# Kernel optimization log

Measured on AMD Instinct MI355X. Metric: run time of the kernel, lower is better.

## Reference

```python
import jax, jax.numpy as jnp
import numpy as np

B, C, T, H, W = 4, 256, 16, 16, 16
C2 = C // 2  # 128


def setup_inputs() -> dict:
    key = jax.random.key(0)
    ks = jax.random.split(key, 12)
    s = 1.0 / np.sqrt(C)
    return {
        "X": jax.random.normal(ks[0], (B, C, T, H, W), dtype=jnp.float32),
        "pe": jax.random.uniform(ks[1], (C, T, H, W), dtype=jnp.float32),
        "task_q": jax.random.uniform(ks[2], (C2, T, H, W), dtype=jnp.float32),
        "task_k": jax.random.uniform(ks[3], (C2, T, H, W), dtype=jnp.float32),
        "task_v": jax.random.uniform(ks[4], (C2, T, H, W), dtype=jnp.float32),
        "Wq": jax.random.normal(ks[5], (C2, C), dtype=jnp.float32) * s,
        "bq": jnp.zeros((C2,), dtype=jnp.float32),
        "Wk": jax.random.normal(ks[6], (C2, C), dtype=jnp.float32) * s,
        "bk": jnp.zeros((C2,), dtype=jnp.float32),
        "Wv": jax.random.normal(ks[7], (C2, C), dtype=jnp.float32) * s,
        "bv": jnp.zeros((C2,), dtype=jnp.float32),
        "Wo": jax.random.normal(ks[8], (C, C2), dtype=jnp.float32) * s,
    }


def reference(X, pe, task_q, task_k, task_v, Wq, bq, Wk, bk, Wv, bv, Wo):
    b, c, t, h, w = X.shape
    c2 = Wq.shape[0]
    n = t * h * w
    Xp = X + pe  # broadcast [C,T,H,W] over batch

    def proj(Wm, bm, task):
        # 1x1x1 Conv3d == channel contraction; add bias and per-task offset
        y = jnp.einsum('bcthw,oc->bothw', Xp, Wm)
        return y + bm[:, None, None, None] + task  # [B,C2,T,H,W]

    q = proj(Wq, bq, task_q).reshape(b, c2, n).transpose(0, 2, 1)  # [B,N,C2]
    k = proj(Wk, bk, task_k).reshape(b, c2, n)                     # [B,C2,N]
    sim = jnp.matmul(q, k)                                         # [B,N,N]
    v = proj(Wv, bv, task_v).reshape(b, c2, n).transpose(0, 2, 1)  # [B,N,C2]
    # NOTE: original torch code computes softmax(sim) but then multiplies by
    # the RAW similarity matrix (softmax output is dead code). Faithful math:
    out = jnp.matmul(sim, v)                                       # [B,N,C2]
    # torch .reshape of contiguous [B,N,C2] -> [B,C2,T,H,W] (layout reinterpret)
    out = out.reshape(b, c2, t, h, w)
    out = jnp.einsum('bcthw,oc->bothw', out, Wo)  # out_conv, no bias
    return out + X
```

## Files before the change

kernel.cpp:

```cpp
#include <hip/hip_runtime.h>
#include <cstddef>

#define BB 4
#define CCH 256
#define C2 128
#define NN 4096
#define PM 384
#define KVS 32

typedef __attribute__((ext_vector_type(8))) short short8v;
typedef __attribute__((ext_vector_type(4))) short short4v;
typedef __attribute__((ext_vector_type(4))) float f32x4;

static __device__ __forceinline__ short f2bf(float f) {
    union { float f; unsigned u; } c; c.f = f;
    unsigned r = (c.u + 0x7FFFu + ((c.u >> 16) & 1u)) >> 16;
    return (short)r;
}

__global__ __launch_bounds__(256) void k_pack(
    const float* __restrict__ Wq, const float* __restrict__ bq,
    const float* __restrict__ Wk, const float* __restrict__ bk,
    const float* __restrict__ Wv, const float* __restrict__ bv,
    short* __restrict__ wpackh, float* __restrict__ bpack)
{
    const int m = blockIdx.x;
    const int c = threadIdx.x;
    const float* w; const float* bs; int mm;
    if (m < C2)        { w = Wq; bs = bq; mm = m; }
    else if (m < 2*C2) { w = Wk; bs = bk; mm = m - C2; }
    else               { w = Wv; bs = bv; mm = m - 2*C2; }
    wpackh[m * CCH + c] = f2bf(w[mm * CCH + c]);
    if (c == 0) bpack[m] = bs[mm];
}

#define LROW 40
__global__ __launch_bounds__(256) void k_projm(
    const float* __restrict__ X, const float* __restrict__ pe,
    const float* __restrict__ tq, const float* __restrict__ tk,
    const float* __restrict__ tv,
    const short* __restrict__ wpackh, const float* __restrict__ bpack,
    float* __restrict__ qkv)
{
    __shared__ short As[128 * LROW];
    __shared__ short Bs[128 * LROW];
    const int b  = blockIdx.z;
    const int m0 = blockIdx.y * 128;
    const int n0 = blockIdx.x * 128;
    const int tid  = threadIdx.x;
    const int wave = tid >> 6;
    const int lane = tid & 63;
    const int lr = lane & 15, lg = lane >> 4;
    const int wm = wave >> 1, wn = wave & 1;
    const float* __restrict__ Xb = X + (size_t)b * CCH * NN;

    const int am  = tid >> 1;
    const int akb = tid & 1;
    const int cq = tid >> 5;
    const int nq = tid & 31;

    f32x4 acc[4][4];
#pragma unroll
    for (int i = 0; i < 4; ++i)
#pragma unroll
        for (int j = 0; j < 4; ++j) acc[i][j] = (f32x4){0.f, 0.f, 0.f, 0.f};

    for (int k0 = 0; k0 < CCH; k0 += 32) {
        {
            const size_t gsrc = (size_t)(m0 + am) * CCH + k0 + akb * 16;
            *(short8v*)&As[am * LROW + akb * 16] =
                *(const short8v*)&wpackh[gsrc];
            *(short8v*)&As[am * LROW + akb * 16 + 8] =
                *(const short8v*)&wpackh[gsrc + 8];
        }
        short sreg[4][4];
#pragma unroll
        for (int j = 0; j < 4; ++j) {
            const int c = k0 + cq * 4 + j;
            const size_t g = (size_t)c * NN + n0 + nq * 4;
            float4 x4 = *(const float4*)&Xb[g];
            float4 p4 = *(const float4*)&pe[g];
            sreg[j][0] = f2bf(x4.x + p4.x);
            sreg[j][1] = f2bf(x4.y + p4.y);
            sreg[j][2] = f2bf(x4.z + p4.z);
            sreg[j][3] = f2bf(x4.w + p4.w);
        }
#pragma unroll
        for (int i = 0; i < 4; ++i) {
            short4v v; v.x = sreg[0][i]; v.y = sreg[1][i]; v.z = sreg[2][i]; v.w = sreg[3][i];
            *(short4v*)&Bs[(nq * 4 + i) * LROW + cq * 4] = v;
        }
        __syncthreads();
        short8v a[4], bfr[4];
#pragma unroll
        for (int fm = 0; fm < 4; ++fm)
            a[fm] = *(const short8v*)&As[(wm * 64 + fm * 16 + lr) * LROW + lg * 8];
#pragma unroll
        for (int fn = 0; fn < 4; ++fn)
            bfr[fn] = *(const short8v*)&Bs[(wn * 64 + fn * 16 + lr) * LROW + lg * 8];
#pragma unroll
        for (int fm = 0; fm < 4; ++fm)
#pragma unroll
            for (int fn = 0; fn < 4; ++fn)
                acc[fm][fn] = __builtin_amdgcn_mfma_f32_16x16x32_bf16(
                    a[fm], bfr[fn], acc[fm][fn], 0, 0, 0);
        __syncthreads();
    }

    const int sel = m0 >> 7;
    const float* __restrict__ task = (sel == 0) ? tq : ((sel == 1) ? tk : tv);
#pragma unroll
    for (int fm = 0; fm < 4; ++fm) {
#pragma unroll
        for (int r = 0; r < 4; ++r) {
            const int m = m0 + wm * 64 + fm * 16 + lg * 4 + r;
            const float bia = bpack[m];
            const int mr = m & (C2 - 1);
#pragma unroll
            for (int fn = 0; fn < 4; ++fn) {
                const int n = n0 + wn * 64 + fn * 16 + lr;
                const float t = task[(size_t)mr * NN + n];
                qkv[((size_t)b * PM + m) * NN + n] = acc[fm][fn][r] + bia + t;
            }
        }
    }
}

__global__ __launch_bounds__(256) void k_kv(
    const float* __restrict__ qkv, float* __restrict__ Mpart)
{
    __shared__ float Ks[64][128];
    __shared__ float Vs[64][128];
    const int b = blockIdx.y;
    const int s = blockIdx.x;
    const int tid = threadIdx.x;
    const int r = tid >> 1;
    const int nb = (tid & 1) * 32;
    const int ti = tid >> 4, tj = tid & 15;
    const float* __restrict__ Kg = qkv + ((size_t)b * PM + C2) * NN;
    const float* __restrict__ Vg = qkv + ((size_t)b * PM + 2 * C2) * NN;
    float acc[8][8];
#pragma unroll
    for (int i = 0; i < 8; ++i)
#pragma unroll
        for (int j = 0; j < 8; ++j) acc[i][j] = 0.f;

    for (int half = 0; half < 2; ++half) {
        const int n0 = s * 128 + half * 64;
#pragma unroll
        for (int q = 0; q < 8; ++q) {
            const int nn = nb + q * 4;
            float4 kv = *(const float4*)&Kg[(size_t)r * NN + n0 + nn];
            Ks[nn+0][r] = kv.x; Ks[nn+1][r] = kv.y; Ks[nn+2][r] = kv.z; Ks[nn+3][r] = kv.w;
            float4 vv = *(const float4*)&Vg[(size_t)r * NN + n0 + nn];
            Vs[nn+0][r] = vv.x; Vs[nn+1][r] = vv.y; Vs[nn+2][r] = vv.z; Vs[nn+3][r] = vv.w;
        }
        __syncthreads();
        for (int nn = 0; nn < 64; ++nn) {
            float4 a0 = *(const float4*)&Ks[nn][ti * 8];
            float4 a1 = *(const float4*)&Ks[nn][ti * 8 + 4];
            float4 b0 = *(const float4*)&Vs[nn][tj * 8];
            float4 b1 = *(const float4*)&Vs[nn][tj * 8 + 4];
            float a[8] = {a0.x, a0.y, a0.z, a0.w, a1.x, a1.y, a1.z, a1.w};
            float v[8] = {b0.x, b0.y, b0.z, b0.w, b1.x, b1.y, b1.z, b1.w};
#pragma unroll
            for (int ii = 0; ii < 8; ++ii)
#pragma unroll
                for (int jj = 0; jj < 8; ++jj)
                    acc[ii][jj] += a[ii] * v[jj];
        }
        __syncthreads();
    }
    float* __restrict__ Mp = Mpart + ((size_t)b * KVS + s) * C2 * C2;
#pragma unroll
    for (int ii = 0; ii < 8; ++ii) {
        const int row = ti * 8 + ii;
        float4 o0, o1;
        o0.x = acc[ii][0]; o0.y = acc[ii][1]; o0.z = acc[ii][2]; o0.w = acc[ii][3];
        o1.x = acc[ii][4]; o1.y = acc[ii][5]; o1.z = acc[ii][6]; o1.w = acc[ii][7];
        *(float4*)&Mp[row * C2 + tj * 8]     = o0;
        *(float4*)&Mp[row * C2 + tj * 8 + 4] = o1;
    }
}

__global__ __launch_bounds__(256) void k_kvred(
    const float* __restrict__ Mpart, float* __restrict__ Mb)
{
    const int b = blockIdx.y;
    const int o = (blockIdx.x * 256 + threadIdx.x) * 4;
    const float* __restrict__ p = Mpart + (size_t)b * KVS * C2 * C2 + o;
    float4 acc;
    acc.x = 0.f; acc.y = 0.f; acc.z = 0.f; acc.w = 0.f;
#pragma unroll 4
    for (int s = 0; s < KVS; ++s) {
        float4 v = *(const float4*)&p[(size_t)s * C2 * C2];
        acc.x += v.x; acc.y += v.y; acc.z += v.z; acc.w += v.w;
    }
    *(float4*)&Mb[(size_t)b * C2 * C2 + o] = acc;
}

__global__ __launch_bounds__(256) void k_qm(
    const float* __restrict__ qkv, const float* __restrict__ Mb,
    float* __restrict__ out3)
{
    __shared__ float Qs[128][64];
    __shared__ float Ms[128][64];
    const int b = blockIdx.z;
    const int nbase = blockIdx.x * 64;
    const int jbase = blockIdx.y * 64;
    const int tid = threadIdx.x;
    const int r = tid >> 1;
    const int cb = (tid & 1) * 32;
    const float* __restrict__ Qg = qkv + (size_t)b * PM * NN;
    const float* __restrict__ Mg = Mb + (size_t)b * C2 * C2;
#pragma unroll
    for (int q = 0; q < 8; ++q) {
        const int cc = cb + q * 4;
        *(float4*)&Qs[r][cc] = *(const float4*)&Qg[(size_t)r * NN + nbase + cc];
        *(float4*)&Ms[r][cc] = *(const float4*)&Mg[r * C2 + jbase + cc];
    }
    __syncthreads();
    const int tn = tid >> 4, tj = tid & 15;
    float acc[4][4];
#pragma unroll
    for (int i = 0; i < 4; ++i)
#pragma unroll
        for (int j = 0; j < 4; ++j) acc[i][j] = 0.f;
    for (int i = 0; i < 128; ++i) {
        float4 a  = *(const float4*)&Qs[i][tn * 4];
        float4 m4 = *(const float4*)&Ms[i][tj * 4];
        float av[4] = {a.x, a.y, a.z, a.w};
        float mv[4] = {m4.x, m4.y, m4.z, m4.w};
#pragma unroll
        for (int ii = 0; ii < 4; ++ii)
#pragma unroll
            for (int jj = 0; jj < 4; ++jj)
                acc[ii][jj] += av[ii] * mv[jj];
    }
#pragma unroll
    for (int ii = 0; ii < 4; ++ii) {
        float4 o;
        o.x = acc[ii][0]; o.y = acc[ii][1]; o.z = acc[ii][2]; o.w = acc[ii][3];
        *(float4*)&out3[((size_t)b * NN + nbase + tn * 4 + ii) * C2 + jbase + tj * 4] = o;
    }
}

__global__ __launch_bounds__(256) void k_final(
    const float* __restrict__ out3, const float* __restrict__ Wo,
    const float* __restrict__ X, float* __restrict__ out)
{
    __shared__ float Ds[64][128];
    __shared__ float Wos[64][128];
    const int g  = blockIdx.x;
    const int o0 = blockIdx.y * 128;
    const int b  = blockIdx.z;
    const int tid = threadIdx.x;
    const int to = tid >> 4, tj = tid & 15;
    float acc[8][8];
#pragma unroll
    for (int i = 0; i < 8; ++i)
#pragma unroll
        for (int j = 0; j < 8; ++j) acc[i][j] = 0.f;

    const float* __restrict__ O3 = out3 + (size_t)b * NN * C2;

    for (int ch = 0; ch < 2; ++ch) {
        const int c0 = ch * 64;
        {
            const int r  = tid >> 2;
            const int jb2 = (tid & 3) * 32;
#pragma unroll
            for (int q = 0; q < 8; ++q) {
                const int j = jb2 + q * 4;
                *(float4*)&Ds[r][j] =
                    *(const float4*)&O3[(size_t)((c0 + r) * 32 + g) * C2 + j];
            }
        }
        {
            const int o  = tid >> 1;
            const int cb2 = (tid & 1) * 32;
#pragma unroll
            for (int q = 0; q < 8; ++q) {
                const int cc = cb2 + q * 4;
                float4 w = *(const float4*)&Wo[(size_t)(o0 + o) * C2 + c0 + cc];
                Wos[cc+0][o] = w.x; Wos[cc+1][o] = w.y;
                Wos[cc+2][o] = w.z; Wos[cc+3][o] = w.w;
            }
        }
        __syncthreads();
#pragma unroll
        for (int cc = 0; cc < 64; ++cc) {
            float4 w0 = *(const float4*)&Wos[cc][to * 8];
            float4 w1 = *(const float4*)&Wos[cc][to * 8 + 4];
            float4 d0 = *(const float4*)&Ds[cc][tj * 8];
            float4 d1 = *(const float4*)&Ds[cc][tj * 8 + 4];
            float w[8] = {w0.x, w0.y, w0.z, w0.w, w1.x, w1.y, w1.z, w1.w};
            float d[8] = {d0.x, d0.y, d0.z, d0.w, d1.x, d1.y, d1.z, d1.w};
#pragma unroll
            for (int ii = 0; ii < 8; ++ii)
#pragma unroll
                for (int jj = 0; jj < 8; ++jj)
                    acc[ii][jj] += w[ii] * d[jj];
        }
        __syncthreads();
    }

    const float* __restrict__ Xb = X + (size_t)b * CCH * NN;
    float* __restrict__ Ob = out + (size_t)b * CCH * NN;
#pragma unroll
    for (int oo = 0; oo < 8; ++oo) {
        const int o = o0 + to * 8 + oo;
        const size_t base = (size_t)o * NN + g * 128 + tj * 8;
        float4 x0 = *(const float4*)&Xb[base];
        float4 x1 = *(const float4*)&Xb[base + 4];
        float4 r0, r1;
        r0.x = acc[oo][0] + x0.x; r0.y = acc[oo][1] + x0.y;
        r0.z = acc[oo][2] + x0.z; r0.w = acc[oo][3] + x0.w;
        r1.x = acc[oo][4] + x1.x; r1.y = acc[oo][5] + x1.y;
        r1.z = acc[oo][6] + x1.z; r1.w = acc[oo][7] + x1.w;
        *(float4*)&Ob[base]     = r0;
        *(float4*)&Ob[base + 4] = r1;
    }
}

extern "C" void kernel_launch(void* const* d_in, const int* in_sizes, int n_in,
                              void* d_out, int out_size, void* d_ws, size_t ws_size,
                              hipStream_t stream) {
    const float* X  = (const float*)d_in[0];
    const float* pe = (const float*)d_in[1];
    const float* tq = (const float*)d_in[2];
    const float* tk = (const float*)d_in[3];
    const float* tv = (const float*)d_in[4];
    const float* Wq = (const float*)d_in[5];
    const float* bq = (const float*)d_in[6];
    const float* Wk = (const float*)d_in[7];
    const float* bk = (const float*)d_in[8];
    const float* Wv = (const float*)d_in[9];
    const float* bv = (const float*)d_in[10];
    const float* Wo = (const float*)d_in[11];
    float* out = (float*)d_out;

    float* ws     = (float*)d_ws;
    float* bpack  = ws;
    short* wpackh = (short*)(ws + 512);
    float* qkv    = ws + 512 + 49152;
    float* Mbuf   = qkv + (size_t)BB * PM * NN;
    float* Mpart  = Mbuf + (size_t)BB * C2 * C2;
    float* out3   = Mpart;

    k_pack<<<dim3(PM), dim3(256), 0, stream>>>(Wq, bq, Wk, bk, Wv, bv, wpackh, bpack);
    k_projm<<<dim3(NN / 128, PM / 128, BB), dim3(256), 0, stream>>>(
        X, pe, tq, tk, tv, wpackh, bpack, qkv);
    k_kv<<<dim3(KVS, BB), dim3(256), 0, stream>>>(qkv, Mpart);
    k_kvred<<<dim3(16, BB), dim3(256), 0, stream>>>(Mpart, Mbuf);
    k_qm<<<dim3(NN / 64, 2, BB), dim3(256), 0, stream>>>(qkv, Mbuf, out3);
    k_final<<<dim3(32, 2, BB), dim3(256), 0, stream>>>(out3, Wo, X, out);
}
```

Measured before the change: 169.7 us.

## Store Q/K/V and intermediates in bf16 and use MFMA for K^T V, QM and output projection

The projection epilogue now writes bf16 Q (transposed to [N,C2]), K and V through a shared-memory staging tile instead of fp32 qkv. The K^T V, Q·M and Wo-projection kernels switch from fp32 FMA loops to bf16 MFMA instructions that read operands directly from global memory, and Wo is packed to bf16 in the pack kernel. The kv split count is halved, and the reduction writes a transposed bf16 M. This cuts memory traffic and moves the matmuls onto matrix cores, but adds bf16 rounding to intermediates and uses uncoalesced scalar gathers in k_final.

```diff
diff --git a/kernel.cpp b/kernel.cpp
--- a/kernel.cpp
+++ b/kernel.cpp
@@ -6,7 +6,7 @@
 #define C2 128
 #define NN 4096
 #define PM 384
-#define KVS 32
+#define KVS 16
 
 typedef __attribute__((ext_vector_type(8))) short short8v;
 typedef __attribute__((ext_vector_type(4))) short short4v;
@@ -22,28 +22,37 @@
     const float* __restrict__ Wq, const float* __restrict__ bq,
     const float* __restrict__ Wk, const float* __restrict__ bk,
     const float* __restrict__ Wv, const float* __restrict__ bv,
-    short* __restrict__ wpackh, float* __restrict__ bpack)
+    const float* __restrict__ Wo,
+    short* __restrict__ wpackh, float* __restrict__ bpack,
+    short* __restrict__ Woh)
 {
     const int m = blockIdx.x;
     const int c = threadIdx.x;
-    const float* w; const float* bs; int mm;
-    if (m < C2)        { w = Wq; bs = bq; mm = m; }
-    else if (m < 2*C2) { w = Wk; bs = bk; mm = m - C2; }
-    else               { w = Wv; bs = bv; mm = m - 2*C2; }
-    wpackh[m * CCH + c] = f2bf(w[mm * CCH + c]);
-    if (c == 0) bpack[m] = bs[mm];
+    if (m < PM) {
+        const float* w; const float* bs; int mm;
+        if (m < C2)        { w = Wq; bs = bq; mm = m; }
+        else if (m < 2*C2) { w = Wk; bs = bk; mm = m - C2; }
+        else               { w = Wv; bs = bv; mm = m - 2*C2; }
+        wpackh[m * CCH + c] = f2bf(w[mm * CCH + c]);
+        if (c == 0) bpack[m] = bs[mm];
+    } else {
+        const int o = m - PM;
+        if (c < C2) Woh[o * C2 + c] = f2bf(Wo[o * C2 + c]);
+    }
 }
 
 #define LROW 40
+#define TSP  136
 __global__ __launch_bounds__(256) void k_projm(
     const float* __restrict__ X, const float* __restrict__ pe,
     const float* __restrict__ tq, const float* __restrict__ tk,
     const float* __restrict__ tv,
     const short* __restrict__ wpackh, const float* __restrict__ bpack,
-    float* __restrict__ qkv)
-{
-    __shared__ short As[128 * LROW];
-    __shared__ short Bs[128 * LROW];
+    short* __restrict__ qt, short* __restrict__ kk, short* __restrict__ vv)
+{
+    __shared__ short smem[17408];
+    short* As = smem;
+    short* Bs = smem + 5120;
     const int b  = blockIdx.z;
     const int m0 = blockIdx.y * 128;
     const int n0 = blockIdx.x * 128;
@@ -56,8 +65,8 @@
 
     const int am  = tid >> 1;
     const int akb = tid & 1;
-    const int cq = tid >> 5;
-    const int nq = tid & 31;
+    const int cq  = tid >> 5;
+    const int nq  = tid & 31;
 
     f32x4 acc[4][4];
 #pragma unroll
@@ -68,10 +77,8 @@
     for (int k0 = 0; k0 < CCH; k0 += 32) {
         {
             const size_t gsrc = (size_t)(m0 + am) * CCH + k0 + akb * 16;
-            *(short8v*)&As[am * LROW + akb * 16] =
-                *(const short8v*)&wpackh[gsrc];
-            *(short8v*)&As[am * LROW + akb * 16 + 8] =
-                *(const short8v*)&wpackh[gsrc + 8];
+            *(short8v*)&As[am * LROW + akb * 16]     = *(const short8v*)&wpackh[gsrc];
+            *(short8v*)&As[am * LROW + akb * 16 + 8] = *(const short8v*)&wpackh[gsrc + 8];
         }
         short sreg[4][4];
 #pragma unroll
@@ -107,220 +114,230 @@
         __syncthreads();
     }
 
+    short* Ts = smem;
     const int sel = m0 >> 7;
-    const float* __restrict__ task = (sel == 0) ? tq : ((sel == 1) ? tk : tv);
-#pragma unroll
-    for (int fm = 0; fm < 4; ++fm) {
-#pragma unroll
-        for (int r = 0; r < 4; ++r) {
-            const int m = m0 + wm * 64 + fm * 16 + lg * 4 + r;
-            const float bia = bpack[m];
-            const int mr = m & (C2 - 1);
+    if (sel == 0) {
+#pragma unroll
+        for (int fm = 0; fm < 4; ++fm)
 #pragma unroll
             for (int fn = 0; fn < 4; ++fn) {
-                const int n = n0 + wn * 64 + fn * 16 + lr;
-                const float t = task[(size_t)mr * NN + n];
-                qkv[((size_t)b * PM + m) * NN + n] = acc[fm][fn][r] + bia + t;
+                const int n_l  = wn * 64 + fn * 16 + lr;
+                const int m_lb = wm * 64 + fm * 16 + lg * 4;
+                short4v v;
+#pragma unroll
+                for (int r = 0; r < 4; ++r) {
+                    const int m_l = m_lb + r;
+                    v[r] = f2bf(acc[fm][fn][r] + bpack[m_l]
+                                + tq[(size_t)m_l * NN + n0 + n_l]);
+                }
+                *(short4v*)&Ts[n_l * TSP + m_lb] = v;
             }
-        }
+        __syncthreads();
+        const int n_l = tid >> 1, half = tid & 1;
+        short* dst = qt + (size_t)b * NN * C2 + (size_t)(n0 + n_l) * C2 + half * 64;
+        const short* src = &Ts[n_l * TSP + half * 64];
+#pragma unroll
+        for (int q2 = 0; q2 < 8; ++q2)
+            *(short8v*)&dst[q2 * 8] = *(const short8v*)&src[q2 * 8];
+    } else {
+        const float* __restrict__ task = (sel == 1) ? tk : tv;
+        short* kv = (sel == 1) ? kk : vv;
+#pragma unroll
+        for (int fm = 0; fm < 4; ++fm)
+#pragma unroll
+            for (int fn = 0; fn < 4; ++fn) {
+                const int n_l = wn * 64 + fn * 16 + lr;
+#pragma unroll
+                for (int r = 0; r < 4; ++r) {
+                    const int m_l = wm * 64 + fm * 16 + lg * 4 + r;
+                    Ts[m_l * TSP + n_l] =
+                        f2bf(acc[fm][fn][r] + bpack[m0 + m_l]
+                             + task[(size_t)m_l * NN + n0 + n_l]);
+                }
+            }
+        __syncthreads();
+        const int m_l = tid >> 1, half = tid & 1;
+        short* dst = kv + (size_t)b * C2 * NN + (size_t)m_l * NN + n0 + half * 64;
+        const short* src = &Ts[m_l * TSP + half * 64];
+#pragma unroll
+        for (int q2 = 0; q2 < 8; ++q2)
+            *(short8v*)&dst[q2 * 8] = *(const short8v*)&src[q2 * 8];
     }
 }
 
 __global__ __launch_bounds__(256) void k_kv(
-    const float* __restrict__ qkv, float* __restrict__ Mpart)
-{
-    __shared__ float Ks[64][128];
-    __shared__ float Vs[64][128];
+    const short* __restrict__ kk, const short* __restrict__ vv,
+    float* __restrict__ Mpart)
+{
+    const int b = blockIdx.y, s = blockIdx.x;
+    const int tid = threadIdx.x;
+    const int wave = tid >> 6, lane = tid & 63;
+    const int lr = lane & 15, lg = lane >> 4;
+    const int wi = wave >> 1, wj = wave & 1;
+    const short* Kb = kk + (size_t)b * C2 * NN;
+    const short* Vb = vv + (size_t)b * C2 * NN;
+    const int nbase = s * 256;
+    f32x4 acc[4][4];
+#pragma unroll
+    for (int i = 0; i < 4; ++i)
+#pragma unroll
+        for (int j = 0; j < 4; ++j) acc[i][j] = (f32x4){0.f, 0.f, 0.f, 0.f};
+
+    for (int ks = 0; ks < 8; ++ks) {
+        const int nn = nbase + ks * 32 + lg * 8;
+        short8v a[4], bv8[4];
+#pragma unroll
+        for (int fi = 0; fi < 4; ++fi)
+            a[fi] = *(const short8v*)&Kb[(size_t)(wi * 64 + fi * 16 + lr) * NN + nn];
+#pragma unroll
+        for (int fj = 0; fj < 4; ++fj)
+            bv8[fj] = *(const short8v*)&Vb[(size_t)(wj * 64 + fj * 16 + lr) * NN + nn];
+#pragma unroll
+        for (int fi = 0; fi < 4; ++fi)
+#pragma unroll
+            for (int fj = 0; fj < 4; ++fj)
+                acc[fi][fj] = __builtin_amdgcn_mfma_f32_16x16x32_bf16(
+                    a[fi], bv8[fj], acc[fi][fj], 0, 0, 0);
+    }
+    float* Mp = Mpart + ((size_t)b * KVS + s) * C2 * C2;
+#pragma unroll
+    for (int fi = 0; fi < 4; ++fi)
+#pragma unroll
+        for (int fj = 0; fj < 4; ++fj) {
+            const int j = wj * 64 + fj * 16 + lr;
+#pragma unroll
+            for (int r = 0; r < 4; ++r) {
+                const int i = wi * 64 + fi * 16 + lg * 4 + r;
+                Mp[(size_t)i * C2 + j] = acc[fi][fj][r];
+            }
+        }
+}
+
+__global__ __launch_bounds__(256) void k_kvred(
+    const float* __restrict__ Mpart, short* __restrict__ Mt)
+{
     const int b = blockIdx.y;
-    const int s = blockIdx.x;
+    const int i = blockIdx.x * 16 + (threadIdx.x >> 4);
+    const int j0 = (threadIdx.x & 15) * 8;
+    const float* p = Mpart + (size_t)b * KVS * C2 * C2 + (size_t)i * C2 + j0;
+    float a8[8];
+#pragma unroll
+    for (int e = 0; e < 8; ++e) a8[e] = 0.f;
+    for (int s = 0; s < KVS; ++s) {
+        float4 v0 = *(const float4*)&p[(size_t)s * C2 * C2];
+        float4 v1 = *(const float4*)&p[(size_t)s * C2 * C2 + 4];
+        a8[0] += v0.x; a8[1] += v0.y; a8[2] += v0.z; a8[3] += v0.w;
+        a8[4] += v1.x; a8[5] += v1.y; a8[6] += v1.z; a8[7] += v1.w;
+    }
+    short* mt = Mt + (size_t)b * C2 * C2;
+#pragma unroll
+    for (int e = 0; e < 8; ++e)
+        mt[(size_t)(j0 + e) * C2 + i] = f2bf(a8[e]);
+}
+
+__global__ __launch_bounds__(256) void k_qm(
+    const short* __restrict__ qt, const short* __restrict__ Mt,
+    short* __restrict__ out3)
+{
+    const int b = blockIdx.y;
+    const int n0 = blockIdx.x * 128;
     const int tid = threadIdx.x;
-    const int r = tid >> 1;
-    const int nb = (tid & 1) * 32;
-    const int ti = tid >> 4, tj = tid & 15;
-    const float* __restrict__ Kg = qkv + ((size_t)b * PM + C2) * NN;
-    const float* __restrict__ Vg = qkv + ((size_t)b * PM + 2 * C2) * NN;
-    float acc[8][8];
-#pragma unroll
-    for (int i = 0; i < 8; ++i)
-#pragma unroll
-        for (int j = 0; j < 8; ++j) acc[i][j] = 0.f;
-
-    for (int half = 0; half < 2; ++half) {
-        const int n0 = s * 128 + half * 64;
-#pragma unroll
-        for (int q = 0; q < 8; ++q) {
-            const int nn = nb + q * 4;
-            float4 kv = *(const float4*)&Kg[(size_t)r * NN + n0 + nn];
-            Ks[nn+0][r] = kv.x; Ks[nn+1][r] = kv.y; Ks[nn+2][r] = kv.z; Ks[nn+3][r] = kv.w;
-            float4 vv = *(const float4*)&Vg[(size_t)r * NN + n0 + nn];
-            Vs[nn+0][r] = vv.x; Vs[nn+1][r] = vv.y; Vs[nn+2][r] = vv.z; Vs[nn+3][r] = vv.w;
-        }
-        __syncthreads();
-        for (int nn = 0; nn < 64; ++nn) {
-            float4 a0 = *(const float4*)&Ks[nn][ti * 8];
-            float4 a1 = *(const float4*)&Ks[nn][ti * 8 + 4];
-            float4 b0 = *(const float4*)&Vs[nn][tj * 8];
-            float4 b1 = *(const float4*)&Vs[nn][tj * 8 + 4];
-            float a[8] = {a0.x, a0.y, a0.z, a0.w, a1.x, a1.y, a1.z, a1.w};
-            float v[8] = {b0.x, b0.y, b0.z, b0.w, b1.x, b1.y, b1.z, b1.w};
-#pragma unroll
-            for (int ii = 0; ii < 8; ++ii)
-#pragma unroll
-                for (int jj = 0; jj < 8; ++jj)
-                    acc[ii][jj] += a[ii] * v[jj];
-        }
-        __syncthreads();
-    }
-    float* __restrict__ Mp = Mpart + ((size_t)b * KVS + s) * C2 * C2;
-#pragma unroll
-    for (int ii = 0; ii < 8; ++ii) {
-        const int row = ti * 8 + ii;
-        float4 o0, o1;
-        o0.x = acc[ii][0]; o0.y = acc[ii][1]; o0.z = acc[ii][2]; o0.w = acc[ii][3];
-        o1.x = acc[ii][4]; o1.y = acc[ii][5]; o1.z = acc[ii][6]; o1.w = acc[ii][7];
-        *(float4*)&Mp[row * C2 + tj * 8]     = o0;
-        *(float4*)&Mp[row * C2 + tj * 8 + 4] = o1;
-    }
-}
-
-__global__ __launch_bounds__(256) void k_kvred(
-    const float* __restrict__ Mpart, float* __restrict__ Mb)
-{
-    const int b = blockIdx.y;
-    const int o = (blockIdx.x * 256 + threadIdx.x) * 4;
-    const float* __restrict__ p = Mpart + (size_t)b * KVS * C2 * C2 + o;
-    float4 acc;
-    acc.x = 0.f; acc.y = 0.f; acc.z = 0.f; acc.w = 0.f;
-#pragma unroll 4
-    for (int s = 0; s < KVS; ++s) {
-        float4 v = *(const float4*)&p[(size_t)s * C2 * C2];
-        acc.x += v.x; acc.y += v.y; acc.z += v.z; acc.w += v.w;
-    }
-    *(float4*)&Mb[(size_t)b * C2 * C2 + o] = acc;
-}
-
-__global__ __launch_bounds__(256) void k_qm(
-    const float* __restrict__ qkv, const float* __restrict__ Mb,
-    float* __restrict__ out3)
-{
-    __shared__ float Qs[128][64];
-    __shared__ float Ms[128][64];
-    const int b = blockIdx.z;
-    const int nbase = blockIdx.x * 64;
-    const int jbase = blockIdx.y * 64;
-    const int tid = threadIdx.x;
-    const int r = tid >> 1;
-    const int cb = (tid & 1) * 32;
-    const float* __restrict__ Qg = qkv + (size_t)b * PM * NN;
-    const float* __restrict__ Mg = Mb + (size_t)b * C2 * C2;
-#pragma unroll
-    for (int q = 0; q < 8; ++q) {
-        const int cc = cb + q * 4;
-        *(float4*)&Qs[r][cc] = *(const float4*)&Qg[(size_t)r * NN + nbase + cc];
-        *(float4*)&Ms[r][cc] = *(const float4*)&Mg[r * C2 + jbase + cc];
-    }
-    __syncthreads();
-    const int tn = tid >> 4, tj = tid & 15;
-    float acc[4][4];
+    const int wave = tid >> 6, lane = tid & 63;
+    const int lr = lane & 15, lg = lane >> 4;
+    const int wj = wave >> 1, wn = wave & 1;
+    const short* Mb = Mt + (size_t)b * C2 * C2;
+    const short* Qb = qt + (size_t)b * NN * C2;
+    f32x4 acc[4][4];
 #pragma unroll
     for (int i = 0; i < 4; ++i)
 #pragma unroll
-        for (int j = 0; j < 4; ++j) acc[i][j] = 0.f;
-    for (int i = 0; i < 128; ++i) {
-        float4 a  = *(const float4*)&Qs[i][tn * 4];
-        float4 m4 = *(const float4*)&Ms[i][tj * 4];
-        float av[4] = {a.x, a.y, a.z, a.w};
-        float mv[4] = {m4.x, m4.y, m4.z, m4.w};
-#pragma unroll
-        for (int ii = 0; ii < 4; ++ii)
-#pragma unroll
-            for (int jj = 0; jj < 4; ++jj)
-                acc[ii][jj] += av[ii] * mv[jj];
-    }
-#pragma unroll
-    for (int ii = 0; ii < 4; ++ii) {
-        float4 o;
-        o.x = acc[ii][0]; o.y = acc[ii][1]; o.z = acc[ii][2]; o.w = acc[ii][3];
-        *(float4*)&out3[((size_t)b * NN + nbase + tn * 4 + ii) * C2 + jbase + tj * 4] = o;
-    }
+        for (int j = 0; j < 4; ++j) acc[i][j] = (f32x4){0.f, 0.f, 0.f, 0.f};
+
+    for (int ks = 0; ks < 4; ++ks) {
+        const int kb = ks * 32 + lg * 8;
+        short8v a[4], bq8[4];
+#pragma unroll
+        for (int fj = 0; fj < 4; ++fj)
+            a[fj] = *(const short8v*)&Mb[(size_t)(wj * 64 + fj * 16 + lr) * C2 + kb];
+#pragma unroll
+        for (int fn = 0; fn < 4; ++fn)
+            bq8[fn] = *(const short8v*)&Qb[(size_t)(n0 + wn * 64 + fn * 16 + lr) * C2 + kb];
+#pragma unroll
+        for (int fj = 0; fj < 4; ++fj)
+#pragma unroll
+            for (int fn = 0; fn < 4; ++fn)
+                acc[fj][fn] = __builtin_amdgcn_mfma_f32_16x16x32_bf16(
+                    a[fj], bq8[fn], acc[fj][fn], 0, 0, 0);
+    }
+    short* O3 = out3 + (size_t)b * NN * C2;
+#pragma unroll
+    for (int fj = 0; fj < 4; ++fj)
+#pragma unroll
+        for (int fn = 0; fn < 4; ++fn) {
+            const int n  = n0 + wn * 64 + fn * 16 + lr;
+            const int jb = wj * 64 + fj * 16 + lg * 4;
+            short4v v;
+#pragma unroll
+            for (int r = 0; r < 4; ++r) v[r] = f2bf(acc[fj][fn][r]);
+            *(short4v*)&O3[(size_t)n * C2 + jb] = v;
+        }
 }
 
 __global__ __launch_bounds__(256) void k_final(
-    const float* __restrict__ out3, const float* __restrict__ Wo,
+    const short* __restrict__ out3, const short* __restrict__ Woh,
     const float* __restrict__ X, float* __restrict__ out)
 {
-    __shared__ float Ds[64][128];
-    __shared__ float Wos[64][128];
     const int g  = blockIdx.x;
     const int o0 = blockIdx.y * 128;
     const int b  = blockIdx.z;
     const int tid = threadIdx.x;
-    const int to = tid >> 4, tj = tid & 15;
-    float acc[8][8];
-#pragma unroll
-    for (int i = 0; i < 8; ++i)
-#pragma unroll
-        for (int j = 0; j < 8; ++j) acc[i][j] = 0.f;
-
-    const float* __restrict__ O3 = out3 + (size_t)b * NN * C2;
-
-    for (int ch = 0; ch < 2; ++ch) {
-        const int c0 = ch * 64;
-        {
-            const int r  = tid >> 2;
-            const int jb2 = (tid & 3) * 32;
-#pragma unroll
-            for (int q = 0; q < 8; ++q) {
-                const int j = jb2 + q * 4;
-                *(float4*)&Ds[r][j] =
-                    *(const float4*)&O3[(size_t)((c0 + r) * 32 + g) * C2 + j];
+    const int wave = tid >> 6, lane = tid & 63;
+    const int lr = lane & 15, lg = lane >> 4;
+    const int wm = wave >> 1, wn = wave & 1;
+    const short* O3 = out3 + (size_t)b * NN * C2;
+    f32x4 acc[4][4];
+#pragma unroll
+    for (int i = 0; i < 4; ++i)
+#pragma unroll
+        for (int j = 0; j < 4; ++j) acc[i][j] = (f32x4){0.f, 0.f, 0.f, 0.f};
+
+    for (int ks = 0; ks < 4; ++ks) {
+        const int c0 = ks * 32;
+        short8v a[4], bb[4];
+#pragma unroll
+        for (int fm = 0; fm < 4; ++fm)
+            a[fm] = *(const short8v*)&Woh[(size_t)(o0 + wm * 64 + fm * 16 + lr) * C2
+                                          + c0 + lg * 8];
+#pragma unroll
+        for (int fn = 0; fn < 4; ++fn) {
+            const int pj = wn * 64 + fn * 16 + lr;
+            short8v t;
+#pragma unroll
+            for (int e = 0; e < 8; ++e)
+                t[e] = O3[(size_t)((c0 + lg * 8 + e) * 32 + g) * C2 + pj];
+            bb[fn] = t;
+        }
+#pragma unroll
+        for (int fm = 0; fm < 4; ++fm)
+#pragma unroll
+            for (int fn = 0; fn < 4; ++fn)
+                acc[fm][fn] = __builtin_amdgcn_mfma_f32_16x16x32_bf16(
+                    a[fm], bb[fn], acc[fm][fn], 0, 0, 0);
+    }
+    const float* Xb = X + (size_t)b * CCH * NN;
+    float* Ob = out + (size_t)b * CCH * NN;
+#pragma unroll
+    for (int fm = 0; fm < 4; ++fm)
+#pragma unroll
+        for (int fn = 0; fn < 4; ++fn) {
+            const int p  = g * 128 + wn * 64 + fn * 16 + lr;
+            const int ob = o0 + wm * 64 + fm * 16 + lg * 4;
+#pragma unroll
+            for (int r = 0; r < 4; ++r) {
+                const size_t ad = (size_t)(ob + r) * NN + p;
+                Ob[ad] = acc[fm][fn][r] + Xb[ad];
             }
         }
-        {
-            const int o  = tid >> 1;
-            const int cb2 = (tid & 1) * 32;
-#pragma unroll
-            for (int q = 0; q < 8; ++q) {
-                const int cc = cb2 + q * 4;
-                float4 w = *(const float4*)&Wo[(size_t)(o0 + o) * C2 + c0 + cc];
-                Wos[cc+0][o] = w.x; Wos[cc+1][o] = w.y;
-                Wos[cc+2][o] = w.z; Wos[cc+3][o] = w.w;
-            }
-        }
-        __syncthreads();
-#pragma unroll
-        for (int cc = 0; cc < 64; ++cc) {
-            float4 w0 = *(const float4*)&Wos[cc][to * 8];
-            float4 w1 = *(const float4*)&Wos[cc][to * 8 + 4];
-            float4 d0 = *(const float4*)&Ds[cc][tj * 8];
-            float4 d1 = *(const float4*)&Ds[cc][tj * 8 + 4];
-            float w[8] = {w0.x, w0.y, w0.z, w0.w, w1.x, w1.y, w1.z, w1.w};
-            float d[8] = {d0.x, d0.y, d0.z, d0.w, d1.x, d1.y, d1.z, d1.w};
-#pragma unroll
-            for (int ii = 0; ii < 8; ++ii)
-#pragma unroll
-                for (int jj = 0; jj < 8; ++jj)
-                    acc[ii][jj] += w[ii] * d[jj];
-        }
-        __syncthreads();
-    }
-
-    const float* __restrict__ Xb = X + (size_t)b * CCH * NN;
-    float* __restrict__ Ob = out + (size_t)b * CCH * NN;
-#pragma unroll
-    for (int oo = 0; oo < 8; ++oo) {
-        const int o = o0 + to * 8 + oo;
-        const size_t base = (size_t)o * NN + g * 128 + tj * 8;
-        float4 x0 = *(const float4*)&Xb[base];
-        float4 x1 = *(const float4*)&Xb[base + 4];
-        float4 r0, r1;
-        r0.x = acc[oo][0] + x0.x; r0.y = acc[oo][1] + x0.y;
-        r0.z = acc[oo][2] + x0.z; r0.w = acc[oo][3] + x0.w;
-        r1.x = acc[oo][4] + x1.x; r1.y = acc[oo][5] + x1.y;
-        r1.z = acc[oo][6] + x1.z; r1.w = acc[oo][7] + x1.w;
-        *(float4*)&Ob[base]     = r0;
-        *(float4*)&Ob[base + 4] = r1;
-    }
 }
 
 extern "C" void kernel_launch(void* const* d_in, const int* in_sizes, int n_in,
@@ -343,16 +360,20 @@
     float* ws     = (float*)d_ws;
     float* bpack  = ws;
     short* wpackh = (short*)(ws + 512);
-    float* qkv    = ws + 512 + 49152;
-    float* Mbuf   = qkv + (size_t)BB * PM * NN;
-    float* Mpart  = Mbuf + (size_t)BB * C2 * C2;
-    float* out3   = Mpart;
-
-    k_pack<<<dim3(PM), dim3(256), 0, stream>>>(Wq, bq, Wk, bk, Wv, bv, wpackh, bpack);
-    k_projm<<<dim3(NN / 128, PM / 128, BB), dim3(256), 0, stream>>>(
-        X, pe, tq, tk, tv, wpackh, bpack, qkv);
-    k_kv<<<dim3(KVS, BB), dim3(256), 0, stream>>>(qkv, Mpart);
-    k_kvred<<<dim3(16, BB), dim3(256), 0, stream>>>(Mpart, Mbuf);
-    k_qm<<<dim3(NN / 64, 2, BB), dim3(256), 0, stream>>>(qkv, Mbuf, out3);
-    k_final<<<dim3(32, 2, BB), dim3(256), 0, stream>>>(out3, Wo, X, out);
-}
+    short* Woh    = (short*)(ws + 512 + 49152);
+    short* qt     = (short*)(ws + 512 + 49152 + 16384);
+    short* kk     = qt + (size_t)BB * NN * C2;
+    short* vv     = kk + (size_t)BB * NN * C2;
+    short* out3   = vv + (size_t)BB * NN * C2;
+    short* Mt     = out3 + (size_t)BB * NN * C2;
+    float* Mpart  = (float*)(Mt + (size_t)BB * C2 * C2);
+
+    k_pack<<<dim3(PM + CCH), dim3(256), 0, stream>>>(
+        Wq, bq, Wk, bk, Wv, bv, Wo, wpackh, bpack, Woh);
+    k_projm<<<dim3(NN / 128, 3, BB), dim3(256), 0, stream>>>(
+        X, pe, tq, tk, tv, wpackh, bpack, qt, kk, vv);
+    k_kv<<<dim3(KVS, BB), dim3(256), 0, stream>>>(kk, vv, Mpart);
+    k_kvred<<<dim3(8, BB), dim3(256), 0, stream>>>(Mpart, Mt);
+    k_qm<<<dim3(NN / 128, BB), dim3(256), 0, stream>>>(qt, Mt, out3);
+    k_final<<<dim3(32, 2, BB), dim3(256), 0, stream>>>(out3, Woh, X, out);
+}
```

After: 139.3 us. 17.9% less time.
